# Optimization experiments

Hardware: AMD Instinct MI355X
Metric: run time of the kernel (lower is better)

The kernel has to match this reference:

```python
import jax, jax.numpy as jnp
import numpy as np

B, T = 32, 32
I, H, O = 8192, 8192, 2048
NNZ_HH, NNZ_IH, NNZ_HO = 1_048_576, 524_288, 262_144


def spmm(rows, cols, vals, n_out, x):
    # COO sparse (n_out, n_in) @ x (n_in, B) -> (n_out, B).
    # Duplicate (row,col) pairs sum, matching torch_sparse.coalesce semantics.
    return jax.ops.segment_sum(vals[:, None] * x[cols], rows, num_segments=n_out)


def setup_inputs() -> dict:
    key = jax.random.key(0)
    ks = jax.random.split(key, 10)
    x = jax.random.normal(ks[0], (B, T, I), jnp.float32)
    hh_rows = jax.random.randint(ks[1], (NNZ_HH,), 0, H)
    hh_cols = jax.random.randint(ks[2], (NNZ_HH,), 0, H)
    hh_vals = jax.random.normal(ks[3], (NNZ_HH,), jnp.float32) * 0.02
    hh_bias = jnp.zeros((H, 1), jnp.float32)
    ih_rows = jax.random.randint(ks[4], (NNZ_IH,), 0, H)
    ih_cols = jax.random.randint(ks[5], (NNZ_IH,), 0, I)
    ih_vals = jax.random.normal(ks[6], (NNZ_IH,), jnp.float32) * 0.02
    ho_rows = jax.random.randint(ks[7], (NNZ_HO,), 0, O)
    ho_cols = jax.random.randint(ks[8], (NNZ_HO,), 0, H)
    ho_vals = jax.random.normal(ks[9], (NNZ_HO,), jnp.float32) * 0.02
    ho_bias = jnp.zeros((O, 1), jnp.float32)
    return dict(x=x, hh_rows=hh_rows, hh_cols=hh_cols, hh_vals=hh_vals,
                hh_bias=hh_bias, ih_rows=ih_rows, ih_cols=ih_cols,
                ih_vals=ih_vals, ho_rows=ho_rows, ho_cols=ho_cols,
                ho_vals=ho_vals, ho_bias=ho_bias)


def reference(x, hh_rows, hh_cols, hh_vals, hh_bias,
              ih_rows, ih_cols, ih_vals,
              ho_rows, ho_cols, ho_vals, ho_bias):
    # batch_first (B, T, I) -> time-major feature-first (T, I, B)
    xs = jnp.transpose(x, (1, 2, 0))
    h0 = jnp.zeros((H, B), x.dtype)  # default_hidden_init_fn='zeros'

    def step(h, x_t):
        pre = (spmm(ih_rows, ih_cols, ih_vals, H, x_t)  # ih (bias_ih=False)
               + spmm(hh_rows, hh_cols, hh_vals, H, h)
               + hh_bias)
        h_new = jax.nn.sigmoid(pre)  # nonlinearity='Sigmoid'
        out_t = spmm(ho_rows, ho_cols, ho_vals, O, h_new) + ho_bias
        return h_new, out_t

    _, outs = jax.lax.scan(step, h0, xs)  # outs: (T, O, B)
    return jnp.transpose(outs, (2, 0, 1))  # (B, T, O)
```

## Files before the change

kernel.cpp:

```cpp
#include <hip/hip_runtime.h>
#include <hip/hip_fp16.h>

constexpr int Bb = 32;
constexpr int Tt = 32;
constexpr int Ii = 8192;
constexpr int Hh = 8192;
constexpr int Oo = 2048;
constexpr int TB = Tt * Bb;
constexpr int TCH = 4;
constexpr int TILE = 2048;
constexpr int FBR = 32;
constexpr int NFB_H = Hh / FBR;
constexpr int NFB_O = Oo / FBR;


__device__ __forceinline__ float entval(uint32_t u) {
  return __half2float(__ushort_as_half((unsigned short)(u >> 16)));
}

__global__ void transpose_x_kernel(const float* __restrict__ x, __half2* __restrict__ x2) {
  int blk = blockIdx.x;
  int tp = blk >> 7;
  int ib = blk & 127;
  int t0 = tp * 2;
  int i0 = ib * 64;
  __shared__ float lds[64][65];
  int tid = threadIdx.x;
  for (int idx = tid; idx < 64 * 64; idx += 256) {
    int row = idx >> 6, il = idx & 63;
    int tt = row >> 5, bb = row & 31;
    lds[il][row] = x[(size_t)bb * Tt * Ii + (size_t)(t0 + tt) * Ii + i0 + il];
  }
  __syncthreads();
  for (int idx = tid; idx < 64 * 32; idx += 256) {
    int il = idx >> 5;
    int q = idx & 31;
    int tt = q >> 4, p = q & 15;
    float lo = lds[il][tt * 32 + 2 * p];
    float hi = lds[il][tt * 32 + 2 * p + 1];
    x2[(size_t)(i0 + il) * (TB / 2) + (size_t)(t0 + tt) * 16 + p] = __floats2half2_rn(lo, hi);
  }
}

__global__ void __launch_bounds__(256) count_kernel(
    const int* __restrict__ r1, int n1, int* __restrict__ tb1, int nt1,
    const int* __restrict__ r2, int n2, int* __restrict__ tb2, int nt2,
    const int* __restrict__ r3, int n3, int* __restrict__ tb3) {
  __shared__ int cnt[NFB_H];
  int tile = blockIdx.x;
  const int* rows; int n; int* tb; int tl; int nfb;
  if (tile < nt1)            { rows = r1; n = n1; tb = tb1; tl = tile;             nfb = NFB_H; }
  else if (tile < nt1 + nt2) { rows = r2; n = n2; tb = tb2; tl = tile - nt1;       nfb = NFB_H; }
  else                       { rows = r3; n = n3; tb = tb3; tl = tile - nt1 - nt2; nfb = NFB_O; }
  for (int i = threadIdx.x; i < nfb; i += 256) cnt[i] = 0;
  __syncthreads();
  int base = tl * TILE;
  for (int k = threadIdx.x; k < TILE; k += 256) {
    int j = base + k;
    if (j < n) atomicAdd(&cnt[rows[j] >> 5], 1);
  }
  __syncthreads();
  for (int i = threadIdx.x; i < nfb; i += 256) tb[tl * nfb + i] = cnt[i];
}

__global__ void __launch_bounds__(256) scan_col_kernel(
    int* __restrict__ tb1, int nt1, int* __restrict__ tb2, int nt2,
    int* __restrict__ tb3, int nt3, int* __restrict__ totals) {
  __shared__ int sums[256];
  int col = blockIdx.x;
  int* tb; int nt; int fb; int nfb;
  if (col < NFB_H)          { tb = tb1; nt = nt1; fb = col;             nfb = NFB_H; }
  else if (col < 2 * NFB_H) { tb = tb2; nt = nt2; fb = col - NFB_H;     nfb = NFB_H; }
  else                      { tb = tb3; nt = nt3; fb = col - 2 * NFB_H; nfb = NFB_O; }
  int tid = threadIdx.x;
  int nper = (nt + 255) >> 8;
  int vals[8];
  int t0 = tid * nper;
  int a = 0;
  for (int i = 0; i < nper; i++) {
    int t = t0 + i;
    vals[i] = (t < nt) ? tb[t * nfb + fb] : 0;
    a += vals[i];
  }
  sums[tid] = a;
  __syncthreads();
  for (int off = 1; off < 256; off <<= 1) {
    int o = (tid >= off) ? sums[tid - off] : 0;
    __syncthreads();
    sums[tid] += o;
    __syncthreads();
  }
  int run = sums[tid] - a;
  for (int i = 0; i < nper; i++) {
    int t = t0 + i;
    if (t < nt) { tb[t * nfb + fb] = run; run += vals[i]; }
  }
  if (tid == 255) totals[col] = sums[255];
}

__global__ void __launch_bounds__(256) scan_base_kernel(
    const int* __restrict__ totals, int* __restrict__ fbb1,
    int* __restrict__ fbb2, int* __restrict__ fbb3) {
  __shared__ int s[256];
  int m = blockIdx.x;
  const int* t; int* fbb; int nfb;
  if (m == 0)      { t = totals;             fbb = fbb1; nfb = NFB_H; }
  else if (m == 1) { t = totals + NFB_H;     fbb = fbb2; nfb = NFB_H; }
  else             { t = totals + 2 * NFB_H; fbb = fbb3; nfb = NFB_O; }
  int tid = threadIdx.x;
  int v = (tid < nfb) ? t[tid] : 0;
  s[tid] = v;
  __syncthreads();
  for (int off = 1; off < 256; off <<= 1) {
    int o = (tid >= off) ? s[tid - off] : 0;
    __syncthreads();
    s[tid] += o;
    __syncthreads();
  }
  if (tid < nfb) fbb[tid] = s[tid] - v;
  if (tid == 255) fbb[nfb] = s[255];
}

__global__ void __launch_bounds__(256) place_kernel(
    const int* __restrict__ r1, const int* __restrict__ c1, const float* __restrict__ v1,
    int n1, const int* __restrict__ tb1, int nt1, const int* __restrict__ fbb1, uint64_t* __restrict__ s1,
    const int* __restrict__ r2, const int* __restrict__ c2, const float* __restrict__ v2,
    int n2, const int* __restrict__ tb2, int nt2, const int* __restrict__ fbb2, uint64_t* __restrict__ s2,
    const int* __restrict__ r3, const int* __restrict__ c3, const float* __restrict__ v3,
    int n3, const int* __restrict__ tb3, const int* __restrict__ fbb3, uint64_t* __restrict__ s3) {
  __shared__ int cnt[NFB_H];
  __shared__ int incl[NFB_H];
  __shared__ uint64_t stg[TILE];
  __shared__ int gad[TILE];
  int tile = blockIdx.x;
  const int* rows; const int* cols; const float* vals; int n;
  const int* tb; const int* fbb; uint64_t* st; int tl; int nfb;
  if (tile < nt1)            { rows = r1; cols = c1; vals = v1; n = n1; tb = tb1; fbb = fbb1; st = s1; tl = tile;             nfb = NFB_H; }
  else if (tile < nt1 + nt2) { rows = r2; cols = c2; vals = v2; n = n2; tb = tb2; fbb = fbb2; st = s2; tl = tile - nt1;       nfb = NFB_H; }
  else                       { rows = r3; cols = c3; vals = v3; n = n3; tb = tb3; fbb = fbb3; st = s3; tl = tile - nt1 - nt2; nfb = NFB_O; }
  int tid = threadIdx.x;
  for (int i = tid; i < NFB_H; i += 256) cnt[i] = 0;
  __syncthreads();
  constexpr int E = TILE / 256;
  uint32_t entv[E]; int rowv[E]; int rnkv[E];
  int base = tl * TILE;
  for (int k = 0; k < E; k++) {
    int j = base + k * 256 + tid;
    if (j < n) {
      int rr = rows[j];
      rowv[k] = rr;
      entv[k] = ((uint32_t)__half_as_ushort(__float2half_rn(vals[j])) << 16) | (uint32_t)cols[j];
      rnkv[k] = atomicAdd(&cnt[rr >> 5], 1);
    } else {
      rowv[k] = -1;
    }
  }
  __syncthreads();
  int v0 = cnt[tid];
  incl[tid] = v0;
  __syncthreads();
  for (int off = 1; off < 256; off <<= 1) {
    int o = (tid >= off) ? incl[tid - off] : 0;
    __syncthreads();
    incl[tid] += o;
    __syncthreads();
  }
  int total = incl[255];
  for (int k = 0; k < E; k++) {
    if (rowv[k] >= 0) {
      int fb = rowv[k] >> 5;
      int slot = (incl[fb] - cnt[fb]) + rnkv[k];
      stg[slot] = ((uint64_t)entv[k] << 32) | (uint32_t)rowv[k];
      gad[slot] = fbb[fb] + tb[tl * nfb + fb] + rnkv[k];
    }
  }
  __syncthreads();
  for (int i = tid; i < total; i += 256) st[gad[i]] = stg[i];
}

__global__ void __launch_bounds__(256) rowcount_kernel(
    const uint64_t* __restrict__ s1, const int* __restrict__ fbb1, int* __restrict__ cu1,
    const uint64_t* __restrict__ s2, const int* __restrict__ fbb2, int* __restrict__ cu2,
    const uint64_t* __restrict__ s3, const int* __restrict__ fbb3, int* __restrict__ cu3) {
  __shared__ int rc[FBR];
  int bx = blockIdx.x;
  const uint64_t* st; const int* fbb; int* cu; int b;
  if (bx < NFB_H)          { st = s1; fbb = fbb1; cu = cu1; b = bx; }
  else if (bx < 2 * NFB_H) { st = s2; fbb = fbb2; cu = cu2; b = bx - NFB_H; }
  else                     { st = s3; fbb = fbb3; cu = cu3; b = bx - 2 * NFB_H; }
  int tid = threadIdx.x;
  if (tid < FBR) rc[tid] = 0;
  __syncthreads();
  int lo = fbb[b], hi = fbb[b + 1];
  for (int j = lo + tid; j < hi; j += 256)
    atomicAdd(&rc[(int)(uint32_t)st[j] & (FBR - 1)], 1);
  __syncthreads();
  if (tid < FBR) cu[(b << 5) + tid] = rc[tid];
}

__global__ void scan_csr_kernel(int* __restrict__ c1, int n1, int* __restrict__ r1,
                                int* __restrict__ c2, int n2, int* __restrict__ r2,
                                int* __restrict__ c3, int n3, int* __restrict__ r3) {
  __shared__ int sums[1024];
  int bx = blockIdx.x;
  int tid = threadIdx.x;
  int* cnt_cursor; int n; int* row_start;
  if (bx == 0)      { cnt_cursor = c1; n = n1; row_start = r1; }
  else if (bx == 1) { cnt_cursor = c2; n = n2; row_start = r2; }
  else              { cnt_cursor = c3; n = n3; row_start = r3; }
  int chunk = (n + 1023) >> 10;
  int base = tid * chunk;
  int s = 0;
  for (int i = 0; i < chunk; i++) {
    int idx = base + i;
    if (idx < n) s += (cnt_cursor[idx] + 7) & ~7;
  }
  sums[tid] = s;
  __syncthreads();
  for (int off = 1; off < 1024; off <<= 1) {
    int other = (tid >= off) ? sums[tid - off] : 0;
    __syncthreads();
    sums[tid] += other;
    __syncthreads();
  }
  int run = sums[tid] - s;
  for (int i = 0; i < chunk; i++) {
    int idx = base + i;
    if (idx < n) {
      int v = cnt_cursor[idx];
      row_start[idx] = run;
      cnt_cursor[idx] = run + v;
      run += (v + 7) & ~7;
    }
  }
  if (tid == 1023) row_start[n] = sums[1023];
}

__global__ void __launch_bounds__(256) csort_kernel(
    const uint64_t* __restrict__ s1, const int* __restrict__ fbb1, const int* __restrict__ rs1, uint32_t* __restrict__ e1,
    const uint64_t* __restrict__ s2, const int* __restrict__ fbb2, const int* __restrict__ rs2, uint32_t* __restrict__ e2,
    const uint64_t* __restrict__ s3, const int* __restrict__ fbb3, const int* __restrict__ rs3, uint32_t* __restrict__ e3) {
  __shared__ uint32_t ob[8192];
  __shared__ int rcnt[FBR];
  __shared__ int rsl[FBR + 1];
  int bx = blockIdx.x;
  const uint64_t* st; const int* fbb; const int* rs; uint32_t* e; int b;
  if (bx < NFB_H)            { st = s1; fbb = fbb1; rs = rs1; e = e1; b = bx; }
  else if (bx < 2 * NFB_H)   { st = s2; fbb = fbb2; rs = rs2; e = e2; b = bx - NFB_H; }
  else                       { st = s3; fbb = fbb3; rs = rs3; e = e3; b = bx - 2 * NFB_H; }
  int tid = threadIdx.x;
  if (tid <= FBR) rsl[tid] = rs[(b << 5) + tid];
  if (tid < FBR) rcnt[tid] = 0;
  __syncthreads();
  int reg0 = rsl[0];
  int rlen = rsl[FBR] - reg0;
  int lo = fbb[b], hi = fbb[b + 1];
  if (rlen <= 8192) {
    for (int i = tid; i < rlen; i += 256) ob[i] = 0;
    __syncthreads();
    for (int j = lo + tid; j < hi; j += 256) {
      uint64_t v = st[j];
      int rl = (int)(uint32_t)v & (FBR - 1);
      int rk = atomicAdd(&rcnt[rl], 1);
      ob[(rsl[rl] - reg0) + rk] = (uint32_t)(v >> 32);
    }
    __syncthreads();
    for (int i = tid; i < rlen; i += 256) e[reg0 + i] = ob[i];
  } else {
    for (int i = tid; i < rlen; i += 256) e[reg0 + i] = 0;
    __syncthreads();
    for (int j = lo + tid; j < hi; j += 256) {
      uint64_t v = st[j];
      int rl = (int)(uint32_t)v & (FBR - 1);
      int rk = atomicAdd(&rcnt[rl], 1);
      e[rsl[rl] + rk] = (uint32_t)(v >> 32);
    }
  }
}

__global__ void __launch_bounds__(256, 8) preih_kernel(
    const int* __restrict__ ih_rs, const int* __restrict__ ih_cur,
    const uint32_t* __restrict__ ih_ent,
    const float* __restrict__ hh_bias, const __half* __restrict__ x2h,
    __half2* __restrict__ preAll) {
  int xcd = blockIdx.x & 7;
  int r = ((blockIdx.x >> 3) << 2) + (threadIdx.x >> 6);
  int lane = threadIdx.x & 63;
  int t0 = xcd * TCH;
  int s0  = __builtin_amdgcn_readfirstlane(ih_rs[r]);
  int cnt = __builtin_amdgcn_readfirstlane(ih_cur[r]) - s0;
  int nb = (cnt + 7) >> 3;
  const int4* ep = (const int4*)(ih_ent + s0);
  const uint32_t* xb = (const uint32_t*)(x2h + (size_t)t0 * Bb);

  float2 a0 = {0.f, 0.f}, a1 = {0.f, 0.f}, a2 = {0.f, 0.f}, a3 = {0.f, 0.f};
  int4 f0 = ep[0], f1 = ep[1];
  for (int i = 0; i < nb; i++) {
    int4 e0 = f0, e1 = f1;
    f0 = ep[2 * i + 2];
    f1 = ep[2 * i + 3];
    uint32_t u0 = (uint32_t)e0.x, u1 = (uint32_t)e0.y, u2 = (uint32_t)e0.z, u3 = (uint32_t)e0.w;
    uint32_t u4 = (uint32_t)e1.x, u5 = (uint32_t)e1.y, u6 = (uint32_t)e1.z, u7 = (uint32_t)e1.w;
    uint32_t g0 = xb[(size_t)(u0 & 0xffff) * (TB / 2) + lane];
    uint32_t g1 = xb[(size_t)(u1 & 0xffff) * (TB / 2) + lane];
    uint32_t g2 = xb[(size_t)(u2 & 0xffff) * (TB / 2) + lane];
    uint32_t g3 = xb[(size_t)(u3 & 0xffff) * (TB / 2) + lane];
    uint32_t g4 = xb[(size_t)(u4 & 0xffff) * (TB / 2) + lane];
    uint32_t g5 = xb[(size_t)(u5 & 0xffff) * (TB / 2) + lane];
    uint32_t g6 = xb[(size_t)(u6 & 0xffff) * (TB / 2) + lane];
    uint32_t g7 = xb[(size_t)(u7 & 0xffff) * (TB / 2) + lane];
    float v0 = entval(u0), v1 = entval(u1), v2 = entval(u2), v3 = entval(u3);
    float v4 = entval(u4), v5 = entval(u5), v6 = entval(u6), v7 = entval(u7);
    float2 x0 = __half22float2(*(__half2*)&g0), x1 = __half22float2(*(__half2*)&g1);
    float2 x2v = __half22float2(*(__half2*)&g2), x3 = __half22float2(*(__half2*)&g3);
    float2 x4 = __half22float2(*(__half2*)&g4), x5 = __half22float2(*(__half2*)&g5);
    float2 x6 = __half22float2(*(__half2*)&g6), x7 = __half22float2(*(__half2*)&g7);
    a0.x += v0 * x0.x;  a0.y += v0 * x0.y;   a0.x += v4 * x4.x;  a0.y += v4 * x4.y;
    a1.x += v1 * x1.x;  a1.y += v1 * x1.y;   a1.x += v5 * x5.x;  a1.y += v5 * x5.y;
    a2.x += v2 * x2v.x; a2.y += v2 * x2v.y;  a2.x += v6 * x6.x;  a2.y += v6 * x6.y;
    a3.x += v3 * x3.x;  a3.y += v3 * x3.y;   a3.x += v7 * x7.x;  a3.y += v7 * x7.y;
  }
  float bias = hh_bias[r];
  float sx = ((a0.x + a1.x) + (a2.x + a3.x)) + bias;
  float sy = ((a0.y + a1.y) + (a2.y + a3.y)) + bias;
  int tt = lane >> 4, p = lane & 15;
  preAll[((size_t)(t0 + tt) * Hh + r) * 16 + p] = __floats2half2_rn(sx, sy);
}

__global__ void __launch_bounds__(256, 8) step_kernel(
    const int* __restrict__ hh_rs, const int* __restrict__ hh_cur,
    const uint32_t* __restrict__ hh_ent,
    const __half* __restrict__ pre_t,
    const __half* __restrict__ hprev,
    __half* __restrict__ hnext) {
  int r = (blockIdx.x * 256 + threadIdx.x) >> 6;
  int lane = threadIdx.x & 63;
  int h = lane >> 5, b = lane & 31;
  int s0  = __builtin_amdgcn_readfirstlane(hh_rs[r]);
  int cnt = __builtin_amdgcn_readfirstlane(hh_cur[r]) - s0;
  int nb = (cnt + 7) >> 3;
  const int4* ep = (const int4*)(hh_ent + s0);
  float pre = __half2float(pre_t[(r << 5) + b]);

  float a0 = 0.f, a1 = 0.f, a2 = 0.f, a3 = 0.f;
  int4 f0 = ep[0], f1 = ep[1];
  for (int i = 0; i < nb; i++) {
    int4 e0 = f0, e1 = f1;
    f0 = ep[2 * i + 2];
    f1 = ep[2 * i + 3];
    uint32_t u0 = (uint32_t)(h ? e0.y : e0.x);
    uint32_t u1 = (uint32_t)(h ? e0.w : e0.z);
    uint32_t u2 = (uint32_t)(h ? e1.y : e1.x);
    uint32_t u3 = (uint32_t)(h ? e1.w : e1.z);
    float h0 = __half2float(hprev[(((size_t)(u0 & 0xffff)) << 5) + b]);
    float h1 = __half2float(hprev[(((size_t)(u1 & 0xffff)) << 5) + b]);
    float h2 = __half2float(hprev[(((size_t)(u2 & 0xffff)) << 5) + b]);
    float h3 = __half2float(hprev[(((size_t)(u3 & 0xffff)) << 5) + b]);
    a0 += entval(u0) * h0;
    a1 += entval(u1) * h1;
    a2 += entval(u2) * h2;
    a3 += entval(u3) * h3;
  }
  float acc = (a0 + a1) + (a2 + a3);
  acc += __shfl_xor(acc, 32, 64);
  float hv = 1.0f / (1.0f + __expf(-(pre + acc)));
  if (h == 0) hnext[(r << 5) + b] = __float2half_rn(hv);
}

__global__ void __launch_bounds__(256, 8) out_kernel(
    const int* __restrict__ ho_rs, const int* __restrict__ ho_cur,
    const uint32_t* __restrict__ ho_ent,
    const float* __restrict__ ho_bias, const __half* __restrict__ hAll,
    float* __restrict__ out_tmp) {
  int xcd = blockIdx.x & 7;
  int w   = (blockIdx.x >> 3) * 4 + (threadIdx.x >> 6);
  int lane = threadIdx.x & 63;
  int h = lane >> 5, b = lane & 31;
  int t0 = xcd * 4;
  constexpr size_t HS = (size_t)Hh * Bb;
  const __half* hbase = hAll + (size_t)(t0 + 1) * HS;

  for (int o = w; o < Oo; o += 1024) {
    int s0  = __builtin_amdgcn_readfirstlane(ho_rs[o]);
    int cnt = __builtin_amdgcn_readfirstlane(ho_cur[o]) - s0;
    int nb = (cnt + 7) >> 3;
    const int4* ep = (const int4*)(ho_ent + s0);
    float bias = (h == 0) ? ho_bias[o] : 0.f;
    float A0 = bias, A1 = bias, A2 = bias, A3 = bias;
    float B0 = 0.f, B1 = 0.f, B2 = 0.f, B3 = 0.f;
    for (int i = 0; i < nb; i++) {
      int4 e0 = ep[2 * i], e1 = ep[2 * i + 1];
      uint32_t u0 = (uint32_t)(h ? e0.y : e0.x);
      uint32_t u1 = (uint32_t)(h ? e0.w : e0.z);
      uint32_t u2 = (uint32_t)(h ? e1.y : e1.x);
      uint32_t u3 = (uint32_t)(h ? e1.w : e1.z);
      const __half* p0 = hbase + (((size_t)(u0 & 0xffff)) << 5) + b;
      const __half* p1 = hbase + (((size_t)(u1 & 0xffff)) << 5) + b;
      const __half* p2 = hbase + (((size_t)(u2 & 0xffff)) << 5) + b;
      const __half* p3 = hbase + (((size_t)(u3 & 0xffff)) << 5) + b;
      float v0 = entval(u0), v1 = entval(u1), v2 = entval(u2), v3 = entval(u3);
      A0 += v0 * __half2float(p0[0]);
      A1 += v0 * __half2float(p0[HS]);
      A2 += v0 * __half2float(p0[2 * HS]);
      A3 += v0 * __half2float(p0[3 * HS]);
      B0 += v1 * __half2float(p1[0]);
      B1 += v1 * __half2float(p1[HS]);
      B2 += v1 * __half2float(p1[2 * HS]);
      B3 += v1 * __half2float(p1[3 * HS]);
      A0 += v2 * __half2float(p2[0]);
      A1 += v2 * __half2float(p2[HS]);
      A2 += v2 * __half2float(p2[2 * HS]);
      A3 += v2 * __half2float(p2[3 * HS]);
      B0 += v3 * __half2float(p3[0]);
      B1 += v3 * __half2float(p3[HS]);
      B2 += v3 * __half2float(p3[2 * HS]);
      B3 += v3 * __half2float(p3[3 * HS]);
    }
    A0 += B0; A1 += B1; A2 += B2; A3 += B3;
    A0 += __shfl_xor(A0, 32, 64);
    A1 += __shfl_xor(A1, 32, 64);
    A2 += __shfl_xor(A2, 32, 64);
    A3 += __shfl_xor(A3, 32, 64);
    if (h == 0) {
      out_tmp[((size_t)(t0 + 0) * Oo + o) * Bb + b] = A0;
      out_tmp[((size_t)(t0 + 1) * Oo + o) * Bb + b] = A1;
      out_tmp[((size_t)(t0 + 2) * Oo + o) * Bb + b] = A2;
      out_tmp[((size_t)(t0 + 3) * Oo + o) * Bb + b] = A3;
    }
  }
}

__global__ void transpose_out_kernel(const float* __restrict__ out_tmp, float* __restrict__ dout) {
  int blk = blockIdx.x;
  int t  = blk >> 5;
  int o0 = (blk & 31) << 6;
  __shared__ float lds[64][33];
  int tid = threadIdx.x;
  for (int idx = tid; idx < 64 * 32; idx += 256) {
    int ol = idx >> 5, bb = idx & 31;
    lds[ol][bb] = out_tmp[(size_t)t * Oo * Bb + (size_t)(o0 + ol) * Bb + bb];
  }
  __syncthreads();
  for (int idx = tid; idx < 32 * 64; idx += 256) {
    int bb = idx >> 6, ol = idx & 63;
    dout[(size_t)bb * Tt * Oo + (size_t)t * Oo + o0 + ol] = lds[ol][bb];
  }
}

extern "C" void kernel_launch(void* const* d_in, const int* in_sizes, int n_in,
                              void* d_out, int out_size, void* d_ws, size_t ws_size,
                              hipStream_t stream) {
  const float* x       = (const float*)d_in[0];
  const int*   hh_rows = (const int*)d_in[1];
  const int*   hh_cols = (const int*)d_in[2];
  const float* hh_vals = (const float*)d_in[3];
  const float* hh_bias = (const float*)d_in[4];
  const int*   ih_rows = (const int*)d_in[5];
  const int*   ih_cols = (const int*)d_in[6];
  const float* ih_vals = (const float*)d_in[7];
  const int*   ho_rows = (const int*)d_in[8];
  const int*   ho_cols = (const int*)d_in[9];
  const float* ho_vals = (const float*)d_in[10];
  const float* ho_bias = (const float*)d_in[11];
  float* out = (float*)d_out;

  const int nnz_hh = in_sizes[1];
  const int nnz_ih = in_sizes[5];
  const int nnz_ho = in_sizes[8];

  const int ntile_ih = (nnz_ih + TILE - 1) / TILE;
  const int ntile_hh = (nnz_hh + TILE - 1) / TILE;
  const int ntile_ho = (nnz_ho + TILE - 1) / TILE;

  char* w = (char*)d_ws;
  size_t off = 0;
  auto alloc = [&](size_t bytes) -> void* {
    void* p = w + off;
    off += (bytes + 255) & ~(size_t)255;
    return p;
  };
  __half* x2h    = (__half*)alloc(2 * (size_t)Ii * TB);
  __half* hAll   = (__half*)alloc(2 * (size_t)(Tt + 1) * Hh * Bb);
  __half* preAll = (__half*)alloc(2 * (size_t)Tt * Hh * Bb);
  float* out_tmp = (float*)alloc(4 * (size_t)Tt * Oo * Bb);
  int*  ih_rs  = (int*)alloc(4 * (size_t)(Hh + 1));
  int*  hh_rs  = (int*)alloc(4 * (size_t)(Hh + 1));
  int*  ho_rs  = (int*)alloc(4 * (size_t)(Oo + 1));
  int*  cur_all = (int*)alloc(4 * (size_t)(Hh + Hh + Oo));
  int*  ih_cur = cur_all;
  int*  hh_cur = cur_all + Hh;
  int*  ho_cur = cur_all + 2 * Hh;
  uint32_t* ih_ent = (uint32_t*)alloc(4 * ((size_t)nnz_ih + 8 * Hh + 64));
  uint32_t* hh_ent = (uint32_t*)alloc(4 * ((size_t)nnz_hh + 8 * Hh + 64));
  uint32_t* ho_ent = (uint32_t*)alloc(4 * ((size_t)nnz_ho + 8 * Oo + 64));
  int* tb_ih  = (int*)alloc(4 * (size_t)(ntile_ih * NFB_H));
  int* tb_hh  = (int*)alloc(4 * (size_t)(ntile_hh * NFB_H));
  int* tb_ho  = (int*)alloc(4 * (size_t)(ntile_ho * NFB_O));
  int* fbb_ih = (int*)alloc(4 * (size_t)(NFB_H + 1));
  int* fbb_hh = (int*)alloc(4 * (size_t)(NFB_H + 1));
  int* fbb_ho = (int*)alloc(4 * (size_t)(NFB_O + 1));
  int* totals = (int*)alloc(4 * (size_t)(2 * NFB_H + NFB_O));

  uint64_t* s_ih = (uint64_t*)preAll;
  uint64_t* s_hh = s_ih + (size_t)nnz_ih;
  uint64_t* s_ho = s_hh + (size_t)nnz_hh;

  hipMemsetAsync(hAll, 0, 2 * (size_t)Hh * Bb, stream);

  transpose_x_kernel<<<(Tt / 2) * (Ii / 64), 256, 0, stream>>>(x, (__half2*)x2h);

  count_kernel<<<ntile_ih + ntile_hh + ntile_ho, 256, 0, stream>>>(
      ih_rows, nnz_ih, tb_ih, ntile_ih,
      hh_rows, nnz_hh, tb_hh, ntile_hh,
      ho_rows, nnz_ho, tb_ho);
  scan_col_kernel<<<2 * NFB_H + NFB_O, 256, 0, stream>>>(
      tb_ih, ntile_ih, tb_hh, ntile_hh, tb_ho, ntile_ho, totals);
  scan_base_kernel<<<3, 256, 0, stream>>>(totals, fbb_ih, fbb_hh, fbb_ho);
  place_kernel<<<ntile_ih + ntile_hh + ntile_ho, 256, 0, stream>>>(
      ih_rows, ih_cols, ih_vals, nnz_ih, tb_ih, ntile_ih, fbb_ih, s_ih,
      hh_rows, hh_cols, hh_vals, nnz_hh, tb_hh, ntile_hh, fbb_hh, s_hh,
      ho_rows, ho_cols, ho_vals, nnz_ho, tb_ho, fbb_ho, s_ho);
  rowcount_kernel<<<2 * NFB_H + NFB_O, 256, 0, stream>>>(
      s_ih, fbb_ih, ih_cur, s_hh, fbb_hh, hh_cur, s_ho, fbb_ho, ho_cur);
  scan_csr_kernel<<<3, 1024, 0, stream>>>(
      ih_cur, Hh, ih_rs, hh_cur, Hh, hh_rs, ho_cur, Oo, ho_rs);
  csort_kernel<<<2 * NFB_H + NFB_O, 256, 0, stream>>>(
      s_ih, fbb_ih, ih_rs, ih_ent,
      s_hh, fbb_hh, hh_rs, hh_ent,
      s_ho, fbb_ho, ho_rs, ho_ent);

  preih_kernel<<<8 * Hh / 4, 256, 0, stream>>>(
      ih_rs, ih_cur, ih_ent, hh_bias, x2h, (__half2*)preAll);

  for (int t = 0; t < Tt; t++) {
    step_kernel<<<Hh / 4, 256, 0, stream>>>(
        hh_rs, hh_cur, hh_ent,
        preAll + (size_t)t * Hh * Bb,
        hAll + (size_t)t * Hh * Bb,
        hAll + (size_t)(t + 1) * Hh * Bb);
  }

  out_kernel<<<2048, 256, 0, stream>>>(
      ho_rs, ho_cur, ho_ent, ho_bias, hAll, out_tmp);
  transpose_out_kernel<<<Tt * (Oo / 64), 256, 0, stream>>>(out_tmp, out);

  (void)n_in; (void)out_size; (void)ws_size;
}
```

Measured before the change: 619.7 us.

## Restructure step kernel for half2 gathers and preih for all timesteps per row

The recurrent step kernel now has each wave split into four 16-lane groups that each process a different int4 of entries and gather half2 (two batch columns) per lane, reducing shuffles via a two-stage xor reduction. Row padding in CSR grows from 8 to 16 entries to fit the 16-entry-per-iteration loop. The preih kernel drops the per-XCD time-chunk split and instead has each wave compute all 32 timesteps of a row, reusing each decoded entry across 8 gathers, with lower occupancy bounds. Padding increases zero work and memory somewhat, and the larger preih register footprint may reduce latency hiding.

```diff
diff --git a/kernel.cpp b/kernel.cpp
--- a/kernel.cpp
+++ b/kernel.cpp
@@ -7,7 +7,6 @@
 constexpr int Hh = 8192;
 constexpr int Oo = 2048;
 constexpr int TB = Tt * Bb;
-constexpr int TCH = 4;
 constexpr int TILE = 2048;
 constexpr int FBR = 32;
 constexpr int NFB_H = Hh / FBR;
@@ -213,7 +212,7 @@
   int s = 0;
   for (int i = 0; i < chunk; i++) {
     int idx = base + i;
-    if (idx < n) s += (cnt_cursor[idx] + 7) & ~7;
+    if (idx < n) s += (cnt_cursor[idx] + 15) & ~15;
   }
   sums[tid] = s;
   __syncthreads();
@@ -230,7 +229,7 @@
       int v = cnt_cursor[idx];
       row_start[idx] = run;
       cnt_cursor[idx] = run + v;
-      run += (v + 7) & ~7;
+      run += (v + 15) & ~15;
     }
   }
   if (tid == 1023) row_start[n] = sums[1023];
@@ -278,53 +277,50 @@
   }
 }
 
-__global__ void __launch_bounds__(256, 8) preih_kernel(
+__global__ void __launch_bounds__(256, 4) preih_kernel(
     const int* __restrict__ ih_rs, const int* __restrict__ ih_cur,
     const uint32_t* __restrict__ ih_ent,
     const float* __restrict__ hh_bias, const __half* __restrict__ x2h,
     __half2* __restrict__ preAll) {
-  int xcd = blockIdx.x & 7;
-  int r = ((blockIdx.x >> 3) << 2) + (threadIdx.x >> 6);
+  int r = blockIdx.x * 4 + (threadIdx.x >> 6);
   int lane = threadIdx.x & 63;
-  int t0 = xcd * TCH;
   int s0  = __builtin_amdgcn_readfirstlane(ih_rs[r]);
   int cnt = __builtin_amdgcn_readfirstlane(ih_cur[r]) - s0;
   int nb = (cnt + 7) >> 3;
   const int4* ep = (const int4*)(ih_ent + s0);
-  const uint32_t* xb = (const uint32_t*)(x2h + (size_t)t0 * Bb);
-
-  float2 a0 = {0.f, 0.f}, a1 = {0.f, 0.f}, a2 = {0.f, 0.f}, a3 = {0.f, 0.f};
+  const uint32_t* xb = (const uint32_t*)x2h;
+
+  float2 a[8];
+  #pragma unroll
+  for (int k = 0; k < 8; k++) a[k] = {0.f, 0.f};
   int4 f0 = ep[0], f1 = ep[1];
   for (int i = 0; i < nb; i++) {
     int4 e0 = f0, e1 = f1;
     f0 = ep[2 * i + 2];
     f1 = ep[2 * i + 3];
-    uint32_t u0 = (uint32_t)e0.x, u1 = (uint32_t)e0.y, u2 = (uint32_t)e0.z, u3 = (uint32_t)e0.w;
-    uint32_t u4 = (uint32_t)e1.x, u5 = (uint32_t)e1.y, u6 = (uint32_t)e1.z, u7 = (uint32_t)e1.w;
-    uint32_t g0 = xb[(size_t)(u0 & 0xffff) * (TB / 2) + lane];
-    uint32_t g1 = xb[(size_t)(u1 & 0xffff) * (TB / 2) + lane];
-    uint32_t g2 = xb[(size_t)(u2 & 0xffff) * (TB / 2) + lane];
-    uint32_t g3 = xb[(size_t)(u3 & 0xffff) * (TB / 2) + lane];
-    uint32_t g4 = xb[(size_t)(u4 & 0xffff) * (TB / 2) + lane];
-    uint32_t g5 = xb[(size_t)(u5 & 0xffff) * (TB / 2) + lane];
-    uint32_t g6 = xb[(size_t)(u6 & 0xffff) * (TB / 2) + lane];
-    uint32_t g7 = xb[(size_t)(u7 & 0xffff) * (TB / 2) + lane];
-    float v0 = entval(u0), v1 = entval(u1), v2 = entval(u2), v3 = entval(u3);
-    float v4 = entval(u4), v5 = entval(u5), v6 = entval(u6), v7 = entval(u7);
-    float2 x0 = __half22float2(*(__half2*)&g0), x1 = __half22float2(*(__half2*)&g1);
-    float2 x2v = __half22float2(*(__half2*)&g2), x3 = __half22float2(*(__half2*)&g3);
-    float2 x4 = __half22float2(*(__half2*)&g4), x5 = __half22float2(*(__half2*)&g5);
-    float2 x6 = __half22float2(*(__half2*)&g6), x7 = __half22float2(*(__half2*)&g7);
-    a0.x += v0 * x0.x;  a0.y += v0 * x0.y;   a0.x += v4 * x4.x;  a0.y += v4 * x4.y;
-    a1.x += v1 * x1.x;  a1.y += v1 * x1.y;   a1.x += v5 * x5.x;  a1.y += v5 * x5.y;
-    a2.x += v2 * x2v.x; a2.y += v2 * x2v.y;  a2.x += v6 * x6.x;  a2.y += v6 * x6.y;
-    a3.x += v3 * x3.x;  a3.y += v3 * x3.y;   a3.x += v7 * x7.x;  a3.y += v7 * x7.y;
+    uint32_t uu[8] = {(uint32_t)e0.x, (uint32_t)e0.y, (uint32_t)e0.z, (uint32_t)e0.w,
+                      (uint32_t)e1.x, (uint32_t)e1.y, (uint32_t)e1.z, (uint32_t)e1.w};
+    #pragma unroll
+    for (int j = 0; j < 8; j++) {
+      uint32_t u = uu[j];
+      const uint32_t* cb = xb + (size_t)(u & 0xffff) * (TB / 2) + lane;
+      float v = entval(u);
+      #pragma unroll
+      for (int k = 0; k < 8; k++) {
+        uint32_t g = cb[k * 64];
+        float2 xv = __half22float2(*(__half2*)&g);
+        a[k].x += v * xv.x;
+        a[k].y += v * xv.y;
+      }
+    }
   }
   float bias = hh_bias[r];
-  float sx = ((a0.x + a1.x) + (a2.x + a3.x)) + bias;
-  float sy = ((a0.y + a1.y) + (a2.y + a3.y)) + bias;
-  int tt = lane >> 4, p = lane & 15;
-  preAll[((size_t)(t0 + tt) * Hh + r) * 16 + p] = __floats2half2_rn(sx, sy);
+  int tq = lane >> 4, p = lane & 15;
+  #pragma unroll
+  for (int k = 0; k < 8; k++) {
+    int t = k * 4 + tq;
+    preAll[((size_t)t * Hh + r) * 16 + p] = __floats2half2_rn(a[k].x + bias, a[k].y + bias);
+  }
 }
 
 __global__ void __launch_bounds__(256, 8) step_kernel(
@@ -335,36 +331,39 @@
     __half* __restrict__ hnext) {
   int r = (blockIdx.x * 256 + threadIdx.x) >> 6;
   int lane = threadIdx.x & 63;
-  int h = lane >> 5, b = lane & 31;
+  int q = lane >> 4, p = lane & 15;
   int s0  = __builtin_amdgcn_readfirstlane(hh_rs[r]);
   int cnt = __builtin_amdgcn_readfirstlane(hh_cur[r]) - s0;
-  int nb = (cnt + 7) >> 3;
+  int nb = (cnt + 15) >> 4;
   const int4* ep = (const int4*)(hh_ent + s0);
-  float pre = __half2float(pre_t[(r << 5) + b]);
-
-  float a0 = 0.f, a1 = 0.f, a2 = 0.f, a3 = 0.f;
-  int4 f0 = ep[0], f1 = ep[1];
+  const uint32_t* hp = (const uint32_t*)hprev;
+  uint32_t pu = ((const uint32_t*)pre_t)[(r << 4) + p];
+  float2 pre2 = __half22float2(*(__half2*)&pu);
+
+  float2 a0 = {0.f, 0.f}, a1 = {0.f, 0.f};
+  int4 f = ep[q];
   for (int i = 0; i < nb; i++) {
-    int4 e0 = f0, e1 = f1;
-    f0 = ep[2 * i + 2];
-    f1 = ep[2 * i + 3];
-    uint32_t u0 = (uint32_t)(h ? e0.y : e0.x);
-    uint32_t u1 = (uint32_t)(h ? e0.w : e0.z);
-    uint32_t u2 = (uint32_t)(h ? e1.y : e1.x);
-    uint32_t u3 = (uint32_t)(h ? e1.w : e1.z);
-    float h0 = __half2float(hprev[(((size_t)(u0 & 0xffff)) << 5) + b]);
-    float h1 = __half2float(hprev[(((size_t)(u1 & 0xffff)) << 5) + b]);
-    float h2 = __half2float(hprev[(((size_t)(u2 & 0xffff)) << 5) + b]);
-    float h3 = __half2float(hprev[(((size_t)(u3 & 0xffff)) << 5) + b]);
-    a0 += entval(u0) * h0;
-    a1 += entval(u1) * h1;
-    a2 += entval(u2) * h2;
-    a3 += entval(u3) * h3;
-  }
-  float acc = (a0 + a1) + (a2 + a3);
-  acc += __shfl_xor(acc, 32, 64);
-  float hv = 1.0f / (1.0f + __expf(-(pre + acc)));
-  if (h == 0) hnext[(r << 5) + b] = __float2half_rn(hv);
+    int4 e = f;
+    f = ep[4 * (i + 1) + q];
+    uint32_t u0 = (uint32_t)e.x, u1 = (uint32_t)e.y, u2 = (uint32_t)e.z, u3 = (uint32_t)e.w;
+    uint32_t g0 = hp[((u0 & 0xffff) << 4) + p];
+    uint32_t g1 = hp[((u1 & 0xffff) << 4) + p];
+    uint32_t g2 = hp[((u2 & 0xffff) << 4) + p];
+    uint32_t g3 = hp[((u3 & 0xffff) << 4) + p];
+    float v0 = entval(u0), v1 = entval(u1), v2 = entval(u2), v3 = entval(u3);
+    float2 x0 = __half22float2(*(__half2*)&g0), x1 = __half22float2(*(__half2*)&g1);
+    float2 x2v = __half22float2(*(__half2*)&g2), x3 = __half22float2(*(__half2*)&g3);
+    a0.x += v0 * x0.x;  a0.y += v0 * x0.y;
+    a1.x += v1 * x1.x;  a1.y += v1 * x1.y;
+    a0.x += v2 * x2v.x; a0.y += v2 * x2v.y;
+    a1.x += v3 * x3.x;  a1.y += v3 * x3.y;
+  }
+  float ax = a0.x + a1.x, ay = a0.y + a1.y;
+  ax += __shfl_xor(ax, 16, 64);  ay += __shfl_xor(ay, 16, 64);
+  ax += __shfl_xor(ax, 32, 64);  ay += __shfl_xor(ay, 32, 64);
+  float hv0 = 1.0f / (1.0f + __expf(-(pre2.x + ax)));
+  float hv1 = 1.0f / (1.0f + __expf(-(pre2.y + ay)));
+  if (q == 0) ((__half2*)hnext)[(r << 4) + p] = __floats2half2_rn(hv0, hv1);
 }
 
 __global__ void __launch_bounds__(256, 8) out_kernel(
@@ -490,9 +489,9 @@
   int*  ih_cur = cur_all;
   int*  hh_cur = cur_all + Hh;
   int*  ho_cur = cur_all + 2 * Hh;
-  uint32_t* ih_ent = (uint32_t*)alloc(4 * ((size_t)nnz_ih + 8 * Hh + 64));
-  uint32_t* hh_ent = (uint32_t*)alloc(4 * ((size_t)nnz_hh + 8 * Hh + 64));
-  uint32_t* ho_ent = (uint32_t*)alloc(4 * ((size_t)nnz_ho + 8 * Oo + 64));
+  uint32_t* ih_ent = (uint32_t*)alloc(4 * ((size_t)nnz_ih + 16 * Hh + 64));
+  uint32_t* hh_ent = (uint32_t*)alloc(4 * ((size_t)nnz_hh + 16 * Hh + 64));
+  uint32_t* ho_ent = (uint32_t*)alloc(4 * ((size_t)nnz_ho + 16 * Oo + 64));
   int* tb_ih  = (int*)alloc(4 * (size_t)(ntile_ih * NFB_H));
   int* tb_hh  = (int*)alloc(4 * (size_t)(ntile_hh * NFB_H));
   int* tb_ho  = (int*)alloc(4 * (size_t)(ntile_ho * NFB_O));
@@ -529,7 +528,7 @@
       s_hh, fbb_hh, hh_rs, hh_ent,
       s_ho, fbb_ho, ho_rs, ho_ent);
 
-  preih_kernel<<<8 * Hh / 4, 256, 0, stream>>>(
+  preih_kernel<<<Hh / 4, 256, 0, stream>>>(
       ih_rs, ih_cur, ih_ent, hh_bias, x2h, (__half2*)preAll);
 
   for (int t = 0; t < Tt; t++) {
```

Measured after the change: 604.6 us. -2.4%, faster.
